# Performance work log

Hardware: AMD Instinct MI355X
Metric: run time of the kernel (lower is better)

## Reference

```python
import jax, jax.numpy as jnp
import numpy as np

REDUCTION_SIZE = 2


def setup_inputs() -> dict:
    key = jax.random.key(0)
    k1, k2 = jax.random.split(key)
    T, E, K, D = 32768, 256, 8, 8  # tokens, experts, top-k, devices
    topk_tensor = jax.random.normal(k1, (1, 1, T, E), dtype=jnp.float32)
    # one-hot expert -> device mapping (contiguous blocks of E//D experts per device)
    dev_of_expert = jnp.arange(E, dtype=jnp.int32) // (E // D)
    expert_mapping = jax.nn.one_hot(dev_of_expert, D, dtype=jnp.int32)[None, None]  # [1,1,E,D]
    expert_metadata = jax.random.randint(k2, (1, 1, T, K), 0, E, dtype=jnp.int32)[None][0]
    return {
        "topk_tensor": topk_tensor,
        "expert_mapping": expert_mapping,
        "expert_metadata": expert_metadata,
    }


def reference(topk_tensor, expert_mapping, expert_metadata):
    r = REDUCTION_SIZE
    topk = topk_tensor[0, 0]          # [T, E] scores over all experts
    mapping = expert_mapping[0, 0]    # [E, D] one-hot expert->device
    meta = expert_metadata[0, 0]      # [T, K] selected expert indices
    T, E = topk.shape
    D = mapping.shape[-1]

    dev_of_expert = jnp.argmax(mapping, axis=-1)            # [E]
    tok_dev = dev_of_expert[meta]                           # [T, K] device of each selected expert

    # token -> device dispatch mask, reduced over groups of `r` tokens
    rows = jnp.arange(T, dtype=jnp.int32)[:, None]
    mask = jnp.zeros((T, D), dtype=jnp.int32).at[rows, tok_dev].set(1)  # [T, D]
    reduced_mask = mask.reshape(T // r, r, D).max(axis=1)               # [T//r, D]

    # selection mask over experts (scatter, avoids [T,K,E] one-hot blowup)
    sel = jnp.zeros((T, E), dtype=topk.dtype).at[rows, meta].set(1.0)   # [T, E]
    gated = topk * sel                                                  # zero non-selected scores

    # remap expert columns into device-local slots
    perm = jnp.argsort(dev_of_expert, stable=True)                      # experts grouped by device
    remapped = gated[:, perm].reshape(T, D, E // D).transpose(1, 0, 2)  # [D, T, E//D]
    return remapped, reduced_mask
```

## Files before the change

kernel.cpp:

```cpp
#include <hip/hip_runtime.h>

#define T_TOK 32768
#define E_EXP 256
#define K_SEL 8
#define D_DEV 8
#define SLOTS (E_EXP / D_DEV)
#define NBLK  1024
#define TOK_PER_BLK (T_TOK / NBLK)
#define TOK_PER_WAVE (TOK_PER_BLK / 4)

__global__ __launch_bounds__(256) void moe_fused_kernel(
    const float* __restrict__ topk, const int* __restrict__ mapping,
    const int* __restrict__ meta, float* __restrict__ out_remap,
    float* __restrict__ out_mask) {
  __shared__ float tile[4][TOK_PER_WAVE * E_EXP];
  __shared__ int sdev[E_EXP];
  __shared__ int spos[E_EXP];
  __shared__ int scnt[4 * D_DEV];

  const int tid  = threadIdx.x;
  const int w    = tid >> 6;
  const int lane = tid & 63;
  const int tbase = blockIdx.x * TOK_PER_BLK + w * TOK_PER_WAVE;
  const int tok   = tbase + (lane >> 3);
  const int e = meta[(size_t)tbase * K_SEL + lane];

  const int4 m0 = ((const int4*)mapping)[tid * 2];
  const int4 m1 = ((const int4*)mapping)[tid * 2 + 1];
  const float4 z4 = {0.f, 0.f, 0.f, 0.f};
#pragma unroll
  for (int i = 0; i < TOK_PER_WAVE; ++i)
    *(float4*)&tile[w][i * E_EXP + lane * 4] = z4;

  {
    int vals[8] = {m0.x, m0.y, m0.z, m0.w, m1.x, m1.y, m1.z, m1.w};
    int best = vals[0], dev = 0;
#pragma unroll
    for (int d = 1; d < 8; ++d)
      if (vals[d] > best) { best = vals[d]; dev = d; }
    sdev[tid] = dev;

    unsigned long long myball = 0ull;
#pragma unroll
    for (int d = 0; d < 8; ++d) {
      unsigned long long b = __ballot(dev == d);
      if (d == dev) myball = b;
      if (lane == d) scnt[w * 8 + d] = __popcll(b);
    }
    const unsigned long long lt = (lane == 0) ? 0ull : (~0ull >> (64 - lane));
    const int lower = __popcll(myball & lt);
    __syncthreads();
    int base = 0;
    for (int d = 0; d < dev; ++d)
      base += scnt[0 * 8 + d] + scnt[1 * 8 + d] + scnt[2 * 8 + d] +
              scnt[3 * 8 + d];
    for (int w2 = 0; w2 < w; ++w2) base += scnt[w2 * 8 + dev];
    spos[tid] = base + lower;
    __syncthreads();
  }

  const float sc = topk[(size_t)tok * E_EXP + e];
  const int pos = spos[e];
  const int dv  = sdev[e];

  unsigned long long bsel = 0ull;
#pragma unroll
  for (int d = 0; d < D_DEV; ++d) {
    unsigned long long b = __ballot(dv == d);
    if ((lane & 7) == d) bsel = b;
  }
  const float fm =
      ((bsel >> (16 * (lane >> 3))) & 0xFFFFull) ? 1.0f : 0.0f;
  if (lane < 32)
    out_mask[(size_t)(tbase >> 1) * D_DEV + lane] = fm;

  tile[w][(lane >> 3) * E_EXP + pos] = sc;

  const int dchunk = lane >> 3;
  const int j      = (lane * 4) & 31;
  float* const obase =
      out_remap + (size_t)dchunk * T_TOK * SLOTS + j;
#pragma unroll
  for (int tt = 0; tt < TOK_PER_WAVE; ++tt) {
    const float4 v = *(const float4*)&tile[w][tt * E_EXP + lane * 4];
    *(float4*)(obase + (size_t)(tbase + tt) * SLOTS) = v;
  }
}

extern "C" void kernel_launch(void* const* d_in, const int* in_sizes, int n_in,
                              void* d_out, int out_size, void* d_ws, size_t ws_size,
                              hipStream_t stream) {
  const float* topk    = (const float*)d_in[0];
  const int*   mapping = (const int*)d_in[1];
  const int*   meta    = (const int*)d_in[2];

  float* out_remap = (float*)d_out;
  float* out_mask  = out_remap + (size_t)D_DEV * T_TOK * SLOTS;

  moe_fused_kernel<<<NBLK, 256, 0, stream>>>(topk, mapping, meta, out_remap,
                                             out_mask);
}
```

Baseline: 85.91 us.

## Use 16-token blocks with padded shared tile and nontemporal coalesced stores

Doubles the grid and halves the tokens per block to 16, so only half the threads gather scores while all 256 threads write out. The shared tile uses padded rows and a mapping that lets each output chunk be written as contiguous 512-byte runs per device, with nontemporal stores and an occupancy hint. The cost it targets is store efficiency and cache pollution from the large output. In exchange it adds a block-wide barrier, leaves half the threads idle during the gather, and repeats the per-block expert-mapping setup twice as often.

```diff
diff --git a/kernel.cpp b/kernel.cpp
--- a/kernel.cpp
+++ b/kernel.cpp
@@ -5,15 +5,17 @@
 #define K_SEL 8
 #define D_DEV 8
 #define SLOTS (E_EXP / D_DEV)
-#define NBLK  1024
-#define TOK_PER_BLK (T_TOK / NBLK)
-#define TOK_PER_WAVE (TOK_PER_BLK / 4)
+#define NBLK  2048
+#define TOK_PER_BLK 16
+#define ROWP 264
 
-__global__ __launch_bounds__(256) void moe_fused_kernel(
+typedef float floatx4 __attribute__((ext_vector_type(4)));
+
+__global__ __launch_bounds__(256, 8) void moe_fused_kernel(
     const float* __restrict__ topk, const int* __restrict__ mapping,
     const int* __restrict__ meta, float* __restrict__ out_remap,
     float* __restrict__ out_mask) {
-  __shared__ float tile[4][TOK_PER_WAVE * E_EXP];
+  __shared__ float tile[TOK_PER_BLK * ROWP];
   __shared__ int sdev[E_EXP];
   __shared__ int spos[E_EXP];
   __shared__ int scnt[4 * D_DEV];
@@ -21,16 +23,21 @@
   const int tid  = threadIdx.x;
   const int w    = tid >> 6;
   const int lane = tid & 63;
-  const int tbase = blockIdx.x * TOK_PER_BLK + w * TOK_PER_WAVE;
-  const int tok   = tbase + (lane >> 3);
-  const int e = meta[(size_t)tbase * K_SEL + lane];
+  const int tbase = blockIdx.x * TOK_PER_BLK;
+
+  int e = 0;
+  if (tid < 128) e = meta[(size_t)tbase * K_SEL + tid];
 
   const int4 m0 = ((const int4*)mapping)[tid * 2];
   const int4 m1 = ((const int4*)mapping)[tid * 2 + 1];
-  const float4 z4 = {0.f, 0.f, 0.f, 0.f};
+
+  const floatx4 z4 = {0.f, 0.f, 0.f, 0.f};
 #pragma unroll
-  for (int i = 0; i < TOK_PER_WAVE; ++i)
-    *(float4*)&tile[w][i * E_EXP + lane * 4] = z4;
+  for (int i = 0; i < 4; ++i) {
+    const int fid = i * 256 + tid;
+    const int a = ((fid >> 3) & 15) * ROWP + (fid >> 7) * SLOTS + (fid & 7) * 4;
+    *(floatx4*)&tile[a] = z4;
+  }
 
   {
     int vals[8] = {m0.x, m0.y, m0.z, m0.w, m1.x, m1.y, m1.z, m1.w};
@@ -59,31 +66,39 @@
     __syncthreads();
   }
 
-  const float sc = topk[(size_t)tok * E_EXP + e];
-  const int pos = spos[e];
-  const int dv  = sdev[e];
+  if (tid < 128) {
+    const int tl  = (w << 3) + (lane >> 3);
+    const float sc = topk[(size_t)(tbase + tl) * E_EXP + e];
+    const int pos = spos[e];
+    const int dv  = sdev[e];
 
-  unsigned long long bsel = 0ull;
+    unsigned long long bsel = 0ull;
 #pragma unroll
-  for (int d = 0; d < D_DEV; ++d) {
-    unsigned long long b = __ballot(dv == d);
-    if ((lane & 7) == d) bsel = b;
+    for (int d = 0; d < D_DEV; ++d) {
+      unsigned long long b = __ballot(dv == d);
+      if ((lane & 7) == d) bsel = b;
+    }
+    if (lane < 32) {
+      const float fm =
+          ((bsel >> (16 * (lane >> 3))) & 0xFFFFull) ? 1.0f : 0.0f;
+      const int rowi = (tbase >> 1) + (w << 2) + (lane >> 3);
+      out_mask[(size_t)rowi * D_DEV + (lane & 7)] = fm;
+    }
+
+    tile[tl * ROWP + pos] = sc;
   }
-  const float fm =
-      ((bsel >> (16 * (lane >> 3))) & 0xFFFFull) ? 1.0f : 0.0f;
-  if (lane < 32)
-    out_mask[(size_t)(tbase >> 1) * D_DEV + lane] = fm;
+  __syncthreads();
 
-  tile[w][(lane >> 3) * E_EXP + pos] = sc;
-
-  const int dchunk = lane >> 3;
-  const int j      = (lane * 4) & 31;
-  float* const obase =
-      out_remap + (size_t)dchunk * T_TOK * SLOTS + j;
 #pragma unroll
-  for (int tt = 0; tt < TOK_PER_WAVE; ++tt) {
-    const float4 v = *(const float4*)&tile[w][tt * E_EXP + lane * 4];
-    *(float4*)(obase + (size_t)(tbase + tt) * SLOTS) = v;
+  for (int i = 0; i < 4; ++i) {
+    const int fid = i * 256 + tid;
+    const int t      = (fid >> 3) & 15;
+    const int dchunk = fid >> 7;
+    const int j      = (fid & 7) * 4;
+    const floatx4 v = *(const floatx4*)&tile[t * ROWP + dchunk * SLOTS + j];
+    float* dst = out_remap + (size_t)dchunk * T_TOK * SLOTS +
+                 (size_t)(tbase + t) * SLOTS + j;
+    __builtin_nontemporal_store(v, (floatx4*)dst);
   }
 }
 
```

Result: no change. 87.40 us (+1.7%).
